# Kernel optimization log

Hardware: AMD Instinct MI355X
Metric: run time of the kernel (lower is better)

## Reference

```python
import jax, jax.numpy as jnp
import numpy as np


def _fir_kernel():
    # StyleGAN-2 low-pass FIR: outer([1,3,3,1]) normalized to sum 1
    k1 = jnp.array([1.0, 3.0, 3.0, 1.0], dtype=jnp.float32)
    k2 = jnp.outer(k1, k1)
    return k2 / k2.sum()


def setup_inputs() -> dict:
    key = jax.random.key(0)
    kx, kw = jax.random.split(key, 2)
    B, H, W, C, OC = 8, 128, 128, 128, 128
    x = jax.random.normal(kx, (B, H, W, C), dtype=jnp.float32)
    conv_w = jax.random.normal(kw, (3, 3, C, OC), dtype=jnp.float32) * 0.02  # HWIO
    conv_b = jnp.zeros((OC,), dtype=jnp.float32)
    return {"x": x, "conv_w": conv_w, "conv_b": conv_b}


def _upsample_fir(x):
    B, H, W, C = x.shape
    kernel = _fir_kernel()
    x_up = jnp.zeros((B, 2 * H, 2 * W, C), dtype=x.dtype)
    x_up = x_up.at[:, ::2, ::2, :].set(x)
    k = jnp.tile(kernel[None, None, :, :], (C, 1, 1, 1))  # OIHW, O=C, I=1
    y = jax.lax.conv_general_dilated(
        jnp.transpose(x_up, (0, 3, 1, 2)),  # NCHW
        k * 4.0,
        window_strides=(1, 1),
        padding="SAME",
        feature_group_count=C,
    )
    return jnp.transpose(y, (0, 2, 3, 1))  # back to NHWC


def reference(x, conv_w, conv_b):
    x_up = _upsample_fir(x)  # (B, 2H, 2W, C)
    out = jax.lax.conv_general_dilated(
        x_up,
        conv_w,
        window_strides=(1, 1),
        padding="SAME",
        dimension_numbers=("NHWC", "HWIO", "NHWC"),
    )
    return out + conv_b
```

## Files before the change

### kernel.cpp

```cpp
#include <hip/hip_runtime.h>

typedef __bf16 bf16x8 __attribute__((ext_vector_type(8)));
typedef float f32x4 __attribute__((ext_vector_type(4)));
typedef unsigned short ushort8 __attribute__((ext_vector_type(8)));

__device__ __forceinline__ unsigned short f2bf(float f) {
  unsigned int u = __builtin_bit_cast(unsigned int, f);
  u += 0x7FFFu + ((u >> 16) & 1u);
  return (unsigned short)(u >> 16);
}

__constant__ float COEF[2][3][3] = {
    {{0.25f, 0.00f, 0.00f},
     {0.75f, 0.75f, 0.25f},
     {0.00f, 0.25f, 0.75f}},
    {{0.75f, 0.25f, 0.00f},
     {0.25f, 0.75f, 0.75f},
     {0.00f, 0.00f, 0.25f}}
};

__global__ void pack_weights(const float* __restrict__ w, unsigned short* __restrict__ pw) {
  const int kt = blockIdx.x >> 3, nt = blockIdx.x & 7;
  const int l = threadIdx.x;
  const int tap = kt >> 2, cblk = kt & 3;
  const int du = tap / 3, dv = tap - du * 3;
  const int c0 = cblk * 32 + ((l >> 4) << 3);
  const int oc = nt * 16 + (l & 15);
  float accp[4][8];
#pragma unroll
  for (int ph = 0; ph < 4; ++ph)
#pragma unroll
    for (int j = 0; j < 8; ++j) accp[ph][j] = 0.0f;
#pragma unroll
  for (int u = 0; u < 3; ++u)
#pragma unroll
    for (int v = 0; v < 3; ++v) {
      const float ra0 = COEF[0][du][u], ra1 = COEF[1][du][u];
      const float cb0 = COEF[0][dv][v], cb1 = COEF[1][dv][v];
      const float c00 = ra0 * cb0, c01 = ra0 * cb1, c10 = ra1 * cb0, c11 = ra1 * cb1;
#pragma unroll
      for (int j = 0; j < 8; ++j) {
        const float wv = w[((u * 3 + v) * 128 + c0 + j) * 128 + oc];
        accp[0][j] += c00 * wv;
        accp[1][j] += c01 * wv;
        accp[2][j] += c10 * wv;
        accp[3][j] += c11 * wv;
      }
    }
  const int fi = ((cblk * 3 + dv) * 3 + du) * 8 + nt;
#pragma unroll
  for (int ph = 0; ph < 4; ++ph) {
    ushort8 o;
#pragma unroll
    for (int j = 0; j < 8; ++j) o[j] = f2bf(accp[ph][j]);
    *(ushort8*)(pw + (((ph * 288 + fi) * 64 + l) << 3)) = o;
  }
}

__global__ __launch_bounds__(256, 2) void fused_all(
    const float* __restrict__ x, const unsigned short* __restrict__ pw,
    const float* __restrict__ w, const float* __restrict__ bias,
    float* __restrict__ out) {
  __shared__ __align__(16) char smem[7 * 19 * 256];

  const int bid = blockIdx.x;
  const int tid = threadIdx.x;

  if (bid < 512) {
    const int chunk = bid & 31;
    const int type = (bid >> 5) & 1;
    const int bi = bid >> 6;
    const int base0 = chunk * 8;
    const float* xb = x + bi * (128 * 128 * 128);

    float* yw = (float*)smem;
    float* part = (float*)(smem + 10240);

    {
      const int c = tid & 127;
      const int sub = tid >> 7;
      for (int k = sub; k < 20; k += 2) {
        const int f = k / 10;
        const int ws = k - f * 10;
        const int t = base0 - 1 + ws;
        float val = 0.0f;
        if ((unsigned)t < 256u) {
          const int t0 = t >> 1;
          const float hA0 = (t & 1) ? 0.25f : 0.75f;
          const float hA1 = 1.0f - hA0;
          const float hF0 = f ? 0.25f : 0.75f;
          const float hF1 = 1.0f - hF0;
          const bool ok = (t0 + 1) < 128;
          if (type == 0) {
            const float v00 = xb[t0 * 128 + c];
            const float v01 = ok ? xb[(t0 + 1) * 128 + c] : 0.0f;
            const float v10 = xb[(128 + t0) * 128 + c];
            const float v11 = ok ? xb[(128 + t0 + 1) * 128 + c] : 0.0f;
            val = hF0 * (hA0 * v00 + hA1 * v01) + hF1 * (hA0 * v10 + hA1 * v11);
          } else {
            const float v00 = xb[(t0 * 128) * 128 + c];
            const float v01 = xb[(t0 * 128 + 1) * 128 + c];
            const float v10 = ok ? xb[((t0 + 1) * 128) * 128 + c] : 0.0f;
            const float v11 = ok ? xb[((t0 + 1) * 128 + 1) * 128 + c] : 0.0f;
            val = hA0 * (hF0 * v00 + hF1 * v01) + hA1 * (hF0 * v10 + hF1 * v11);
          }
        }
        yw[(f * 10 + ws) * 128 + c] = val;
      }
    }
    __syncthreads();

    const int wv = tid >> 6;
    const int oc0 = (tid & 63) * 2;
    const int cbase = wv * 32;

    float acc[8][2] = {};
#pragma unroll 1
    for (int cc = 0; cc < 32; ++cc) {
      float yr[2][10];
#pragma unroll
      for (int f = 0; f < 2; ++f)
#pragma unroll
        for (int ws = 0; ws < 10; ++ws)
          yr[f][ws] = yw[(f * 10 + ws) * 128 + cbase + cc];
#pragma unroll
      for (int tf = 0; tf < 2; ++tf) {
#pragma unroll
        for (int tb = 0; tb < 3; ++tb) {
          const int uu = (type == 0) ? (tf + 1) : tb;
          const int vv = (type == 0) ? tb : (tf + 1);
          const float2 w2 = *(const float2*)(
              w + ((uu * 3 + vv) * 128 + cbase + cc) * 128 + oc0);
#pragma unroll
          for (int pos = 0; pos < 8; ++pos) {
            const float yv = yr[tf][pos + tb];
            acc[pos][0] += yv * w2.x;
            acc[pos][1] += yv * w2.y;
          }
        }
      }
    }

#pragma unroll
    for (int pos = 0; pos < 8; ++pos)
      *(float2*)(part + (wv * 8 + pos) * 128 + oc0) = *(float2*)acc[pos];
    __syncthreads();

    const int pos = tid >> 5;
    const int ocp = (tid & 31) * 4;
    float4 s = {0.f, 0.f, 0.f, 0.f};
#pragma unroll
    for (int w4i = 0; w4i < 4; ++w4i) {
      const float4 v = *(const float4*)(part + (w4i * 8 + pos) * 128 + ocp);
      s.x += v.x; s.y += v.y; s.z += v.z; s.w += v.w;
    }
    const int posg = base0 + pos;
    if (!(type == 1 && posg == 0)) {
      const int p = (type == 0) ? 0 : posg;
      const int q = (type == 0) ? posg : 0;
      const float4 b4 = *(const float4*)(bias + ocp);
      float4 r;
      r.x = s.x + b4.x; r.y = s.y + b4.y; r.z = s.z + b4.z; r.w = s.w + b4.w;
      *(float4*)(out + bi * (256 * 256 * 128) + (p * 256 + q) * 128 + ocp) = r;
    }
    return;
  }

  char* xlds = smem;
  const int o = bid - 512;
  const int blk = (o & 7) * 256 + (o >> 3);
  const int bimg = blk >> 8;
  const int it = (blk >> 3) & 31;
  const int jt = blk & 7;
  const int I0 = it * 4, J0 = jt * 16;
  const float* xb = x + bimg * (128 * 128 * 128);

  const int lane = tid & 63;
  const int l15 = lane & 15;
  const int lh = lane >> 4;
  const int wid = tid >> 6;
  const int a = wid >> 1;
  const int b = wid & 1;
  const int ph = a * 2 + b;

  const char* pwb = (const char*)pw + ph * 294912 + lane * 16;

#define LOADB(buf, g_, du_)                                           \
  do {                                                                \
    const char* bp_ = pwb + (((g_) * 3 + (du_)) << 13);               \
    _Pragma("unroll") for (int n = 0; n < 8; ++n)                     \
        buf[n] = *(const bf16x8*)(bp_ + n * 1024);                    \
  } while (0)

  bf16x8 bX[8], bY[8];
  LOADB(bX, 0, 0);

  for (int idx = tid; idx < 7 * 19 * 16; idx += 256) {
    const int cp = idx & 15;
    const int pos = idx >> 4;
    const int xr = pos / 19;
    const int xc = pos - xr * 19;
    const int gi = I0 - 1 + xr;
    const int gj = J0 - 1 + xc;
    ushort8 u8 = {};
    if (((unsigned)gi < 128u) && ((unsigned)gj < 128u)) {
      const float* p = xb + ((gi << 7) + gj) * 128 + (cp << 3);
      const float4 A = *(const float4*)p;
      const float4 Bv = *(const float4*)(p + 4);
      u8[0] = f2bf(A.x); u8[1] = f2bf(A.y); u8[2] = f2bf(A.z); u8[3] = f2bf(A.w);
      u8[4] = f2bf(Bv.x); u8[5] = f2bf(Bv.y); u8[6] = f2bf(Bv.z); u8[7] = f2bf(Bv.w);
    }
    int byte = (pos << 8) + (cp << 4);
    byte ^= (pos & 7) << 4;
    *(ushort8*)(xlds + byte) = u8;
  }
  __syncthreads();

  f32x4 acc[4][8] = {};
  const int colpart = l15 + b;

#define AREAD(rr, dv_)                                                \
  do {                                                                \
    const int posa = (a + (rr)) * 19 + colpart + (dv_);               \
    int byte_ = (posa << 8) + kbyte;                                  \
    byte_ ^= (posa & 7) << 4;                  \
    af[rr] = *(const bf16x8*)(xlds + byte_);                          \
  } while (0)

#define MFMAS(du_, buf)                                               \
  do {                                                                \
    __builtin_amdgcn_s_setprio(1);                                    \
    _Pragma("unroll") for (int m = 0; m < 4; ++m)                     \
        _Pragma("unroll") for (int n = 0; n < 8; ++n)                 \
            acc[m][n] = __builtin_amdgcn_mfma_f32_16x16x32_bf16(      \
                af[(du_) + m], buf[n], acc[m][n], 0, 0, 0);           \
    __builtin_amdgcn_s_setprio(0);                                    \
  } while (0)

#pragma unroll 1
  for (int g = 0; g < 12; g += 2) {
    {
      const int cblk = (g * 11) >> 5;
      const int dv = g - cblk * 3;
      const int kbyte = (cblk * 4 + lh) << 4;
      bf16x8 af[6];
      AREAD(0, dv); AREAD(1, dv); AREAD(2, dv);
      AREAD(3, dv); AREAD(4, dv); AREAD(5, dv);
      LOADB(bY, g, 1);
      MFMAS(0, bX);
      LOADB(bX, g, 2);
      MFMAS(1, bY);
      LOADB(bY, g + 1, 0);
      MFMAS(2, bX);
    }
    {
      const int g1 = g + 1;
      const int cblk = (g1 * 11) >> 5;
      const int dv = g1 - cblk * 3;
      const int kbyte = (cblk * 4 + lh) << 4;
      bf16x8 af[6];
      AREAD(0, dv); AREAD(1, dv); AREAD(2, dv);
      AREAD(3, dv); AREAD(4, dv); AREAD(5, dv);
      LOADB(bX, g1, 1);
      MFMAS(0, bY);
      LOADB(bY, g1, 2);
      MFMAS(1, bX);
      {
        const int gn = (g + 2 < 12) ? (g + 2) : 11;
        LOADB(bX, gn, 0);
      }
      MFMAS(2, bY);
    }
  }
#undef AREAD
#undef MFMAS
#undef LOADB

  float bv[8];
#pragma unroll
  for (int n = 0; n < 8; ++n) bv[n] = bias[n * 16 + l15];
  float* ob = out + bimg * (256 * 256 * 128) + l15;
#pragma unroll
  for (int m = 0; m < 4; ++m) {
    const int p = it * 8 + 2 * m + a;
    if (p == 0) continue;
#pragma unroll
    for (int jr = 0; jr < 4; ++jr) {
      const int q = jt * 32 + 2 * (lh * 4 + jr) + b;
      if (q == 0) continue;
      float* orow = ob + (p * 256 + q) * 128;
#pragma unroll
      for (int n = 0; n < 8; ++n) orow[n * 16] = acc[m][n][jr] + bv[n];
    }
  }
}

extern "C" void kernel_launch(void* const* d_in, const int* in_sizes, int n_in,
                              void* d_out, int out_size, void* d_ws, size_t ws_size,
                              hipStream_t stream) {
  const float* x = (const float*)d_in[0];
  const float* w = (const float*)d_in[1];
  const float* bias = (const float*)d_in[2];
  float* out = (float*)d_out;
  unsigned short* pw = (unsigned short*)d_ws;

  pack_weights<<<dim3(288), dim3(64), 0, stream>>>(w, pw);
  fused_all<<<dim3(2560), dim3(256), 0, stream>>>(x, pw, w, bias, out);
}
```

Baseline: 178.1 us.

## Split output channels across blocks to raise occupancy in conv kernel

Each interior block now computes half of the output channels (64 instead of 128), which halves the accumulator and B-fragment register footprint and doubles the interior grid to 4096 blocks. Launch bounds are raised to 3 blocks per SM, and the B-fragment pipeline becomes a three-buffer, single-step loop. The LDS swizzle is widened from 8 to 16 positions to reduce bank conflicts. The cost is that every block now loads and converts the input tile twice, and each A fragment is reused across fewer MFMAs.

```diff
diff --git a/kernel.cpp b/kernel.cpp
--- a/kernel.cpp
+++ b/kernel.cpp
@@ -57,7 +57,7 @@
   }
 }
 
-__global__ __launch_bounds__(256, 2) void fused_all(
+__global__ __launch_bounds__(256, 3) void fused_all(
     const float* __restrict__ x, const unsigned short* __restrict__ pw,
     const float* __restrict__ w, const float* __restrict__ bias,
     float* __restrict__ out) {
@@ -168,10 +168,11 @@
 
   char* xlds = smem;
   const int o = bid - 512;
-  const int blk = (o & 7) * 256 + (o >> 3);
-  const int bimg = blk >> 8;
-  const int it = (blk >> 3) & 31;
-  const int jt = blk & 7;
+  const int blk = (o & 7) * 512 + (o >> 3);
+  const int bimg = blk >> 9;
+  const int it = (blk >> 4) & 31;
+  const int jt = (blk >> 1) & 7;
+  const int och = blk & 1;
   const int I0 = it * 4, J0 = jt * 16;
   const float* xb = x + bimg * (128 * 128 * 128);
 
@@ -183,17 +184,17 @@
   const int b = wid & 1;
   const int ph = a * 2 + b;
 
-  const char* pwb = (const char*)pw + ph * 294912 + lane * 16;
+  const char* pwb = (const char*)pw + ph * 294912 + och * 4096 + lane * 16;
 
 #define LOADB(buf, g_, du_)                                           \
   do {                                                                \
     const char* bp_ = pwb + (((g_) * 3 + (du_)) << 13);               \
-    _Pragma("unroll") for (int n = 0; n < 8; ++n)                     \
+    _Pragma("unroll") for (int n = 0; n < 4; ++n)                     \
         buf[n] = *(const bf16x8*)(bp_ + n * 1024);                    \
   } while (0)
 
-  bf16x8 bX[8], bY[8];
-  LOADB(bX, 0, 0);
+  bf16x8 b0[4], b1[4], b2[4];
+  LOADB(b0, 0, 0);
 
   for (int idx = tid; idx < 7 * 19 * 16; idx += 256) {
     const int cp = idx & 15;
@@ -211,78 +212,63 @@
       u8[4] = f2bf(Bv.x); u8[5] = f2bf(Bv.y); u8[6] = f2bf(Bv.z); u8[7] = f2bf(Bv.w);
     }
     int byte = (pos << 8) + (cp << 4);
-    byte ^= (pos & 7) << 4;
+    byte ^= (pos & 15) << 4;
     *(ushort8*)(xlds + byte) = u8;
   }
   __syncthreads();
 
-  f32x4 acc[4][8] = {};
+  f32x4 acc[4][4] = {};
   const int colpart = l15 + b;
 
-#define AREAD(rr, dv_)                                                \
+#define AREAD(rr, dv_, kbyte_)                                        \
   do {                                                                \
     const int posa = (a + (rr)) * 19 + colpart + (dv_);               \
-    int byte_ = (posa << 8) + kbyte;                                  \
-    byte_ ^= (posa & 7) << 4;                  \
+    int byte_ = (posa << 8) + (kbyte_);                               \
+    byte_ ^= (posa & 15) << 4;   \
     af[rr] = *(const bf16x8*)(xlds + byte_);                          \
   } while (0)
 
 #define MFMAS(du_, buf)                                               \
   do {                                                                \
     __builtin_amdgcn_s_setprio(1);                                    \
-    _Pragma("unroll") for (int m = 0; m < 4; ++m)                     \
-        _Pragma("unroll") for (int n = 0; n < 8; ++n)                 \
-            acc[m][n] = __builtin_amdgcn_mfma_f32_16x16x32_bf16(      \
-                af[(du_) + m], buf[n], acc[m][n], 0, 0, 0);           \
+    _Pragma("unroll") for (int mt = 0; mt < 4; ++mt)                  \
+        _Pragma("unroll") for (int n = 0; n < 4; ++n)                 \
+            acc[mt][n] = __builtin_amdgcn_mfma_f32_16x16x32_bf16(     \
+                af[(du_) + mt], buf[n], acc[mt][n], 0, 0, 0);         \
     __builtin_amdgcn_s_setprio(0);                                    \
   } while (0)
 
 #pragma unroll 1
-  for (int g = 0; g < 12; g += 2) {
+  for (int g = 0; g < 12; ++g) {
+    const int cblk = (g * 11) >> 5;
+    const int dv = g - cblk * 3;
+    const int kbyte = (cblk * 4 + lh) << 4;
+
+    bf16x8 af[6];
+    AREAD(0, dv, kbyte); AREAD(1, dv, kbyte); AREAD(2, dv, kbyte);
+    AREAD(3, dv, kbyte); AREAD(4, dv, kbyte); AREAD(5, dv, kbyte);
+
+    LOADB(b1, g, 1);
+    MFMAS(0, b0);
+    LOADB(b2, g, 2);
+    MFMAS(1, b1);
     {
-      const int cblk = (g * 11) >> 5;
-      const int dv = g - cblk * 3;
-      const int kbyte = (cblk * 4 + lh) << 4;
-      bf16x8 af[6];
-      AREAD(0, dv); AREAD(1, dv); AREAD(2, dv);
-      AREAD(3, dv); AREAD(4, dv); AREAD(5, dv);
-      LOADB(bY, g, 1);
-      MFMAS(0, bX);
-      LOADB(bX, g, 2);
-      MFMAS(1, bY);
-      LOADB(bY, g + 1, 0);
-      MFMAS(2, bX);
-    }
-    {
-      const int g1 = g + 1;
-      const int cblk = (g1 * 11) >> 5;
-      const int dv = g1 - cblk * 3;
-      const int kbyte = (cblk * 4 + lh) << 4;
-      bf16x8 af[6];
-      AREAD(0, dv); AREAD(1, dv); AREAD(2, dv);
-      AREAD(3, dv); AREAD(4, dv); AREAD(5, dv);
-      LOADB(bX, g1, 1);
-      MFMAS(0, bY);
-      LOADB(bY, g1, 2);
-      MFMAS(1, bX);
-      {
-        const int gn = (g + 2 < 12) ? (g + 2) : 11;
-        LOADB(bX, gn, 0);
-      }
-      MFMAS(2, bY);
-    }
+      const int gn = (g < 11) ? (g + 1) : 11;
+      LOADB(b0, gn, 0);
+    }
+    MFMAS(2, b2);
   }
 #undef AREAD
 #undef MFMAS
 #undef LOADB
 
-  float bv[8];
-#pragma unroll
-  for (int n = 0; n < 8; ++n) bv[n] = bias[n * 16 + l15];
-  float* ob = out + bimg * (256 * 256 * 128) + l15;
-#pragma unroll
-  for (int m = 0; m < 4; ++m) {
-    const int p = it * 8 + 2 * m + a;
+  float bv[4];
+#pragma unroll
+  for (int n = 0; n < 4; ++n) bv[n] = bias[och * 64 + n * 16 + l15];
+  float* ob = out + bimg * (256 * 256 * 128) + och * 64 + l15;
+#pragma unroll
+  for (int mt = 0; mt < 4; ++mt) {
+    const int p = it * 8 + 2 * mt + a;
     if (p == 0) continue;
 #pragma unroll
     for (int jr = 0; jr < 4; ++jr) {
@@ -290,7 +276,7 @@
       if (q == 0) continue;
       float* orow = ob + (p * 256 + q) * 128;
 #pragma unroll
-      for (int n = 0; n < 8; ++n) orow[n * 16] = acc[m][n][jr] + bv[n];
+      for (int n = 0; n < 4; ++n) orow[n * 16] = acc[mt][n][jr] + bv[n];
     }
   }
 }
@@ -305,5 +291,5 @@
   unsigned short* pw = (unsigned short*)d_ws;
 
   pack_weights<<<dim3(288), dim3(64), 0, stream>>>(w, pw);
-  fused_all<<<dim3(2560), dim3(256), 0, stream>>>(x, pw, w, bias, out);
-}
+  fused_all<<<dim3(4608), dim3(256), 0, stream>>>(x, pw, w, bias, out);
+}
```

Result: slower. 202.9 us (+13.9%).
